# Kernel tuning notes

Hardware: AMD Instinct MI355X
Metric: run time of the kernel (lower is better)

## Reference

```python
import jax, jax.numpy as jnp
import numpy as np

# Hyperparameters (from TopoGradLoss.__init__)
K_KDE = 32      # neighbors for the Gaussian KDE density estimate
K_RIPS = 16     # neighbors defining the Rips (k-NN) graph
SCALE = 64.0    # Gaussian kernel bandwidth (squared-distance scale)
DESTNUM = 10    # number of salient persistence pairs to preserve
N, D = 8192, 32


def setup_inputs() -> dict:
    key = jax.random.key(0)
    x = jax.random.normal(key, (N, D), dtype=jnp.float32)
    return {"x": x}


def _kde_and_rips(x):
    # Full pairwise squared distances [N, N] (memory-bound traffic)
    sq = jnp.sum(x * x, axis=1)
    d2 = jnp.maximum(sq[:, None] + sq[None, :] - 2.0 * (x @ x.T), 0.0)
    # KDE density from the K_KDE nearest neighbors (self included, exp(0))
    neg_knn, _ = jax.lax.top_k(-d2, K_KDE)          # negated smallest sq-dists
    kde = jnp.exp(neg_knn / SCALE).sum(axis=1)       # sum_j exp(-||xi-xj||^2/scale)
    kde = kde / kde.max()                            # normalize to max density 1
    # Rips graph: K_RIPS nearest-neighbor indices
    _, rips_idxs = jax.lax.top_k(-d2, K_RIPS)
    return kde, rips_idxs


def _persistence_pairs(kde, rips_idxs):
    # ToMATo-style 0-dim persistence of the superlevel-set filtration of kde
    # on the k-NN Rips graph. Process points in decreasing density; each new
    # point either starts a cluster or merges clusters, killing all but the
    # densest root. death[r] = index of the point at which cluster born at r dies.
    n = kde.shape[0]
    order = jnp.argsort(-kde)     # decreasing density
    rank = jnp.argsort(order)     # rank[i] = filtration position of point i

    def step(carry, i):
        root, death = carry
        nbr = rips_idxs[i]                          # [K_RIPS]
        valid = rank[nbr] < rank[i]                 # neighbors already in filtration
        nroot = root[nbr]                           # their current cluster roots
        scores = jnp.where(valid, kde[nroot], -jnp.inf)
        g = jnp.where(valid.any(), nroot[jnp.argmax(scores)], i)  # surviving root
        # roots that die at point i (merged into g)
        dying = jnp.where(valid & (nroot != g), nroot, n)
        death = death.at[dying].set(i, mode="drop")
        # re-root every point whose root got merged
        merge_from = jnp.where(valid, nroot, -1)
        member = (root[:, None] == merge_from[None, :]).any(axis=1)
        root = jnp.where(member, g, root).at[i].set(g)
        return (root, death), None

    root0 = jnp.arange(n)
    death0 = jnp.full((n,), -1, dtype=jnp.int32)
    (root, death), _ = jax.lax.scan(step, (root0, death0), order)
    # essential pair: global density mode paired with the global minimum
    death = death.at[order[0]].set(jnp.argmin(kde).astype(death.dtype))
    return death


def _loss(kde, death):
    valid = death >= 0
    dvals = kde[jnp.clip(death, 0)]                 # death densities
    pers = kde - dvals                              # persistence per birth index
    masked = jnp.where(valid, jax.lax.stop_gradient(pers), -jnp.inf)
    _, top_idx = jax.lax.top_k(masked, DESTNUM)     # DESTNUM most persistent pairs
    salient = jnp.zeros(kde.shape[0], dtype=bool).at[top_idx].set(True)
    changing = valid & ~salient
    # collapse spurious pairs to zero persistence
    l_change = jnp.sum(jnp.where(changing, pers ** 2, 0.0))
    # push salient pairs toward maximal saliency (birth=1, death=0)
    l_salient = jnp.sum(jnp.where(valid & salient, (kde - 1.0) ** 2 + dvals ** 2, 0.0))
    return l_change + l_salient


def reference(x):
    kde, rips_idxs = _kde_and_rips(x)
    # pairing is combinatorial: piecewise-constant w.r.t. x (stop-gradient),
    # matching the custom autograd Function's gradient semantics
    death = _persistence_pairs(jax.lax.stop_gradient(kde), rips_idxs)
    return _loss(kde, death)
```

## Files before the change

kernel.cpp:

```cpp
#include <hip/hip_runtime.h>
#include <hip/hip_bf16.h>

#define NPTS 8192
#define DIM 32
#define KKDE 32
#define KRIPS 16
#define DESTNUM 10

__device__ __forceinline__ unsigned long long shfl_xor_u64(unsigned long long v, int m) {
  int lo = __shfl_xor((int)(unsigned)(v & 0xFFFFFFFFull), m, 64);
  int hi = __shfl_xor((int)(unsigned)(v >> 32), m, 64);
  return (((unsigned long long)(unsigned)hi) << 32) | (unsigned)lo;
}

template <int CTRL>
__device__ __forceinline__ int dpp_mov(int v) {
  return __builtin_amdgcn_update_dpp(0, v, CTRL, 0xF, 0xF, false);
}
__device__ __forceinline__ int row_max16(int v) {
  int t;
  t = dpp_mov<0x128>(v); v = (t > v) ? t : v;
  t = dpp_mov<0x124>(v); v = (t > v) ? t : v;
  t = dpp_mov<0x122>(v); v = (t > v) ? t : v;
  t = dpp_mov<0x121>(v); v = (t > v) ? t : v;
  return v;
}
__device__ __forceinline__ int row_min16(int v) {
  int t;
  t = dpp_mov<0x128>(v); v = (t < v) ? t : v;
  t = dpp_mov<0x124>(v); v = (t < v) ? t : v;
  t = dpp_mov<0x122>(v); v = (t < v) ? t : v;
  t = dpp_mov<0x121>(v); v = (t < v) ? t : v;
  return v;
}
__device__ __forceinline__ int wave_sum64(int c) {
  int t;
  t = dpp_mov<0x128>(c); c += t;
  t = dpp_mov<0x124>(c); c += t;
  t = dpp_mov<0x122>(c); c += t;
  t = dpp_mov<0x121>(c); c += t;
  return __builtin_amdgcn_readlane(c, 0) + __builtin_amdgcn_readlane(c, 16) +
         __builtin_amdgcn_readlane(c, 32) + __builtin_amdgcn_readlane(c, 48);
}

__global__ __launch_bounds__(64) void detect_kernel(const unsigned short* __restrict__ x,
                                                    int* __restrict__ flag) {
  int lane = threadIdx.x;
  unsigned u = x[2 * lane];
  int e = (u >> 7) & 0xFF;
  bool pass = (e >= 110 && e <= 130);
  unsigned long long b = __ballot(pass);
  if (lane == 0) flag[0] = (__popcll(b) >= 32) ? 1 : 0;
}

__global__ __launch_bounds__(256) void tr_kernel(const unsigned short* __restrict__ xh,
                                                 const int* __restrict__ flag,
                                                 float* __restrict__ xT) {
  int e = blockIdx.x * 256 + threadIdx.x;
  if (e >= NPTS * DIM) return;
  int p = e >> 5, q = e & 31;
  float v;
  if (flag[0] != 0) v = __uint_as_float(((unsigned)xh[e]) << 16);
  else v = ((const float*)xh)[e];
  xT[q * NPTS + p] = v;
}

__device__ __forceinline__ void topk_emit(const unsigned* K, const int i, const int w,
                                          const int lane, const int t,
                                          unsigned long long* cand, unsigned long long* srt,
                                          unsigned long long* fin, float* knnv, int* knni,
                                          float* __restrict__ kde, int* __restrict__ rips) {
  unsigned lo = 0u, hi = 0x7F800000u;
  int chi = 2048;
  while (chi > 64 && (hi - lo) > 3u) {
    const unsigned span = hi - lo;
    const unsigned t1 = lo + (span >> 2);
    const unsigned t2 = lo + (span >> 1);
    int c = 0;
#pragma unroll
    for (int e = 0; e < 32; ++e) {
      unsigned a = (K[e] <= t2) ? 0x10000u : 0u;
      a = (K[e] <= t1) ? 0x10001u : a;
      c += (int)a;
    }
    const int tot = wave_sum64(c);
    const int c1 = tot & 0xFFFF;
    const int c2 = (int)((unsigned)tot >> 16);
    if (c1 >= 32) { hi = t1; chi = c1; }
    else if (c2 >= 32) { lo = t1; hi = t2; chi = c2; }
    else lo = t2;
  }
  while (chi > 64 && (hi - lo) > 1u) {
    const unsigned mid = lo + ((hi - lo) >> 1);
    int c = 0;
#pragma unroll
    for (int e = 0; e < 32; ++e) c += (K[e] <= mid) ? 1 : 0;
    const int tot = wave_sum64(c);
    if (tot >= 32) { hi = mid; chi = tot; } else lo = mid;
  }
  cand[(w << 6) | lane] = ~0ull;
  const unsigned long long below = (lane == 0) ? 0ull : (~0ull >> (64 - lane));
  int base = 0;
#pragma unroll
  for (int e = 0; e < 32; ++e) {
    const bool sel = (K[e] <= hi);
    const unsigned long long b = __ballot(sel);
    if (sel) {
      const int pos = base + __popcll(b & below);
      if (pos < 64) {
        const int col = ((((w << 9) + ((e >> 2) << 6) + lane)) << 2) + (e & 3);
        cand[(w << 6) + pos] = (((unsigned long long)K[e]) << 32) | (unsigned)col;
      }
    }
    base += __popcll(b);
  }
  unsigned long long v = cand[(w << 6) | lane];
#pragma unroll
  for (int k = 2; k <= 64; k <<= 1) {
#pragma unroll
    for (int j = 32; j > 0; j >>= 1) {
      if (j >= k) continue;
      unsigned long long o = shfl_xor_u64(v, j);
      bool keepMin = (((lane & k) == 0) == ((lane & j) == 0));
      v = keepMin ? (v < o ? v : o) : (v > o ? v : o);
    }
  }
  if (lane < 32) srt[(w << 5) | lane] = v;
  __syncthreads();
  if (w < 2) {
    const unsigned long long* A = &srt[(w * 2) << 5];
    const unsigned long long* B = &srt[(w * 2 + 1) << 5];
    unsigned long long m = (lane < 32) ? A[lane] : B[63 - lane];
#pragma unroll
    for (int j = 32; j > 0; j >>= 1) {
      unsigned long long o = shfl_xor_u64(m, j);
      bool keepMin = ((lane & j) == 0);
      m = keepMin ? (m < o ? m : o) : (m > o ? m : o);
    }
    if (lane < 32) fin[(w << 5) | lane] = m;
  }
  __syncthreads();
  if (w == 0) {
    unsigned long long m = (lane < 32) ? fin[lane] : fin[32 + (63 - lane)];
#pragma unroll
    for (int j = 32; j > 0; j >>= 1) {
      unsigned long long o = shfl_xor_u64(m, j);
      bool keepMin = ((lane & j) == 0);
      m = keepMin ? (m < o ? m : o) : (m > o ? m : o);
    }
    if (lane < 32) {
      knnv[lane] = __uint_as_float((unsigned)(m >> 32));
      knni[lane] = (int)(m & 0x1FFFull);
    }
  }
  __syncthreads();
  if (t == 0) {
    float s = 0.f;
    for (int k = 0; k < KKDE; ++k) s += expf(knnv[k] * -0.015625f);
    kde[i] = s;
  }
  if (t < KRIPS) rips[i * KRIPS + t] = knni[t];
}

__global__ __launch_bounds__(256) void dist_kernel(const float* __restrict__ xT,
                                                   float* __restrict__ Dc,
                                                   int c0) {
  __shared__ float ax[DIM][128];
  __shared__ float bx[DIM][128];
  __shared__ float sqS[128];
  __shared__ float sS[128];
  const int t = threadIdx.x;
  const int i0 = c0 + blockIdx.y * 128;
  const int j0 = blockIdx.x * 128;
  for (int e = t; e < DIM * 128; e += 256) {
    int q = e >> 7, l = e & 127;
    ax[q][l] = xT[q * NPTS + i0 + l];
    bx[q][l] = xT[q * NPTS + j0 + l];
  }
  __syncthreads();
  {
    const int l = t & 127;
    const float* col = (t < 128) ? &ax[0][l] : &bx[0][l];
    float s = 0.f;
#pragma unroll
    for (int q = 0; q < DIM; ++q) s = fmaf(col[q * 128], col[q * 128], s);
    if (t < 128) sqS[l] = s;
    else sS[l] = s;
  }
  __syncthreads();
  const int tr = (t >> 4) << 3;
  const int tc = (t & 15) << 3;
  float acc[8][8];
#pragma unroll
  for (int a = 0; a < 8; ++a)
#pragma unroll
    for (int b = 0; b < 8; ++b) acc[a][b] = 0.f;
#pragma unroll 4
  for (int q = 0; q < DIM; ++q) {
    float4 a0 = *(const float4*)&ax[q][tr];
    float4 a1 = *(const float4*)&ax[q][tr + 4];
    float4 b0 = *(const float4*)&bx[q][tc];
    float4 b1 = *(const float4*)&bx[q][tc + 4];
    float ar[8] = {a0.x, a0.y, a0.z, a0.w, a1.x, a1.y, a1.z, a1.w};
    float br[8] = {b0.x, b0.y, b0.z, b0.w, b1.x, b1.y, b1.z, b1.w};
#pragma unroll
    for (int a = 0; a < 8; ++a)
#pragma unroll
      for (int b = 0; b < 8; ++b) acc[a][b] = fmaf(ar[a], br[b], acc[a][b]);
  }
#pragma unroll
  for (int a = 0; a < 8; ++a) {
    const float sqi = sqS[tr + a];
    float4 o0, o1;
    o0.x = fmaxf(fmaf(-2.f, acc[a][0], sqi + sS[tc + 0]), 0.f);
    o0.y = fmaxf(fmaf(-2.f, acc[a][1], sqi + sS[tc + 1]), 0.f);
    o0.z = fmaxf(fmaf(-2.f, acc[a][2], sqi + sS[tc + 2]), 0.f);
    o0.w = fmaxf(fmaf(-2.f, acc[a][3], sqi + sS[tc + 3]), 0.f);
    o1.x = fmaxf(fmaf(-2.f, acc[a][4], sqi + sS[tc + 4]), 0.f);
    o1.y = fmaxf(fmaf(-2.f, acc[a][5], sqi + sS[tc + 5]), 0.f);
    o1.z = fmaxf(fmaf(-2.f, acc[a][6], sqi + sS[tc + 6]), 0.f);
    o1.w = fmaxf(fmaf(-2.f, acc[a][7], sqi + sS[tc + 7]), 0.f);
    float* dst = Dc + (size_t)(i0 - c0 + tr + a) * NPTS + (j0 + tc);
    *(float4*)dst = o0;
    *(float4*)(dst + 4) = o1;
  }
}

__global__ __launch_bounds__(256) void select_kernel(const float* __restrict__ Dc,
                                                     float* __restrict__ kde,
                                                     int* __restrict__ rips,
                                                     int c0) {
  __shared__ unsigned long long cand[4 * 64];
  __shared__ unsigned long long srt[4 * 32];
  __shared__ unsigned long long fin[64];
  __shared__ float knnv[KKDE];
  __shared__ int knni[KKDE];
  const int i = c0 + blockIdx.x;
  const int t = threadIdx.x;
  const int w = t >> 6, lane = t & 63;
  const float4* D4 = (const float4*)(Dc + (size_t)blockIdx.x * NPTS);
  unsigned K[32];
#pragma unroll
  for (int s = 0; s < 8; ++s) {
    float4 v = D4[(w << 9) + (s << 6) + lane];
    K[4 * s + 0] = __float_as_uint(v.x);
    K[4 * s + 1] = __float_as_uint(v.y);
    K[4 * s + 2] = __float_as_uint(v.z);
    K[4 * s + 3] = __float_as_uint(v.w);
  }
  topk_emit(K, i, w, lane, t, cand, srt, fin, knnv, knni, kde, rips);
}

__global__ __launch_bounds__(256) void knn_kernel(const float* __restrict__ xT,
                                                  float* __restrict__ kde,
                                                  int* __restrict__ rips) {
  __shared__ unsigned long long cand[4 * 64];
  __shared__ unsigned long long srt[4 * 32];
  __shared__ unsigned long long fin[64];
  __shared__ float knnv[KKDE];
  __shared__ int knni[KKDE];
  __shared__ float xis[DIM];
  const int i = blockIdx.x;
  const int t = threadIdx.x;
  const int w = t >> 6, lane = t & 63;
  if (t < DIM) xis[t] = xT[t * NPTS + i];
  __syncthreads();
  float xi[DIM];
#pragma unroll
  for (int q = 0; q < DIM; ++q) xi[q] = xis[q];
  float sqi = 0.f;
#pragma unroll
  for (int q = 0; q < DIM; ++q) sqi = fmaf(xi[q], xi[q], sqi);
  const float4* xT4 = (const float4*)xT;
  unsigned K[32];
#pragma unroll
  for (int s = 0; s < 8; ++s) {
    const int j4 = (w << 9) + (s << 6) + lane;
    float d0 = 0.f, d1 = 0.f, d2 = 0.f, d3 = 0.f;
    float s0 = 0.f, s1 = 0.f, s2 = 0.f, s3 = 0.f;
#pragma unroll
    for (int q = 0; q < DIM; ++q) {
      float4 v = xT4[q * (NPTS / 4) + j4];
      const float xq = xi[q];
      d0 = fmaf(xq, v.x, d0); s0 = fmaf(v.x, v.x, s0);
      d1 = fmaf(xq, v.y, d1); s1 = fmaf(v.y, v.y, s1);
      d2 = fmaf(xq, v.z, d2); s2 = fmaf(v.z, v.z, s2);
      d3 = fmaf(xq, v.w, d3); s3 = fmaf(v.w, v.w, s3);
    }
    K[4 * s + 0] = __float_as_uint(fmaxf(fmaf(-2.f, d0, sqi + s0), 0.f));
    K[4 * s + 1] = __float_as_uint(fmaxf(fmaf(-2.f, d1, sqi + s1), 0.f));
    K[4 * s + 2] = __float_as_uint(fmaxf(fmaf(-2.f, d2, sqi + s2), 0.f));
    K[4 * s + 3] = __float_as_uint(fmaxf(fmaf(-2.f, d3, sqi + s3), 0.f));
  }
  topk_emit(K, i, w, lane, t, cand, srt, fin, knnv, knni, kde, rips);
}

__global__ __launch_bounds__(256) void prep_kernel(float* __restrict__ kde,
                                                   int* __restrict__ death,
                                                   int* __restrict__ scali) {
  __shared__ float red[256];
  __shared__ unsigned long long red64[256];
  __shared__ float kmaxS;
  const int t = threadIdx.x;
  float m = 0.f;
  for (int p = t; p < NPTS; p += 256) m = fmaxf(m, kde[p]);
  red[t] = m;
  __syncthreads();
  for (int s = 128; s; s >>= 1) {
    if (t < s) red[t] = fmaxf(red[t], red[t + s]);
    __syncthreads();
  }
  if (t == 0) kmaxS = red[0];
  __syncthreads();
  const float km = kmaxS;
  unsigned long long best = ~0ull;
  for (int p = t; p < NPTS; p += 256) {
    float v = kde[p] / km;
    kde[p] = v;
    death[p] = -1;
    unsigned long long kk = (((unsigned long long)__float_as_uint(v)) << 32) | (unsigned)p;
    if (kk < best) best = kk;
  }
  red64[t] = best;
  __syncthreads();
  for (int s = 128; s; s >>= 1) {
    if (t < s && red64[t + s] < red64[t]) red64[t] = red64[t + s];
    __syncthreads();
  }
  if (t == 0) scali[0] = (int)(red64[0] & 0xFFFFFFFFull);
}

__global__ __launch_bounds__(1024) void sort_kernel(const float* __restrict__ kde,
                                                    int* __restrict__ order,
                                                    int* __restrict__ rankp) {
  __shared__ float kv[NPTS];
  __shared__ unsigned short ki[NPTS];
  int t = threadIdx.x;
  for (int p = t; p < NPTS; p += 1024) { kv[p] = kde[p]; ki[p] = (unsigned short)p; }
  __syncthreads();
  for (int size = 2; size <= NPTS; size <<= 1) {
    for (int stride = size >> 1; stride > 0; stride >>= 1) {
      for (int q = t; q < NPTS / 2; q += 1024) {
        int lo = ((q & ~(stride - 1)) << 1) | (q & (stride - 1));
        int hi = lo + stride;
        float va = kv[lo], vb = kv[hi];
        int ia = ki[lo], ib = ki[hi];
        bool aFirst = (va > vb) || (va == vb && ia < ib);
        bool up = ((lo & size) == 0);
        if (up != aFirst) {
          kv[lo] = vb; kv[hi] = va;
          ki[lo] = (unsigned short)ib; ki[hi] = (unsigned short)ia;
        }
      }
      __syncthreads();
    }
  }
  for (int p = t; p < NPTS; p += 1024) {
    int idx = ki[p];
    order[p] = idx;
    rankp[idx] = p;
  }
}

__global__ __launch_bounds__(256) void onbr_kernel(const int* __restrict__ order,
                                                   const int* __restrict__ rankp,
                                                   const int* __restrict__ rips,
                                                   unsigned short* __restrict__ onbr) {
  int e = blockIdx.x * 256 + threadIdx.x;
  if (e >= NPTS * KRIPS) return;
  int t = e >> 4, kk = e & 15;
  int i = order[t];
  int nbr = rips[i * KRIPS + kk];
  int r = rankp[nbr];
  unsigned short v = (unsigned short)r;
  if (r < t) {
    v |= 0x8000;
    if ((r >> 4) == (t >> 4)) v |= 0x4000;
  }
  onbr[e] = v;
}

__global__ __launch_bounds__(64) void scan_kernel(const int* __restrict__ order,
                                                  const unsigned short* __restrict__ onbr,
                                                  int* __restrict__ death,
                                                  const int* __restrict__ scali) {
  __shared__ unsigned short rootR[NPTS];
  __shared__ unsigned short orderS[NPTS];
  const int lane = threadIdx.x;
  for (int p = lane; p < NPTS; p += 64) {
    rootR[p] = (unsigned short)p;
    orderS[p] = (unsigned short)order[p];
  }
  __syncthreads();
  const int sub = lane >> 4;

  auto process = [&](unsigned short D, int pref, int posBase, bool& cln) {
    const int nbr = D & 0x1FFF;
    const bool valid = (D & 0x8000) != 0;
    const bool hz = (D & 0x4000) != 0;
    int rd = cln ? pref : (int)rootR[nbr];
    const int rv = row_max16(valid ? rd : -1);
    const bool uniOk = !valid || (rd == rv);
    const unsigned long long uniB = __ballot(uniOk);
    const unsigned long long hzB = __ballot(hz);
    const unsigned long long badB = (~uniB) | hzB;
    if (badB == 0ull) {
      if ((lane & 15) == 0 && rv >= 0) rootR[posBase + sub] = (unsigned short)rv;
      return;
    }
    const int sstar = (__ffsll(badB) - 1) >> 4;
    if ((lane & 15) == 0 && sub < sstar && rv >= 0)
      rootR[posBase + sub] = (unsigned short)rv;
    cln = false;
    if (hzB != 0ull) {
      const int f = (int)rootR[nbr];
      rd = hz ? f : rd;
    }
    {
      const bool fwd2 = hz && (nbr >= posBase + sstar);
      const int rv2 = row_max16(valid ? rd : -1);
      const unsigned long long bad2 = __ballot(fwd2 || (valid && rd != rv2));
      if (bad2 == 0ull) {
        if ((lane & 15) == 0 && sub >= sstar && rv2 >= 0)
          rootR[posBase + sub] = (unsigned short)rv2;
        return;
      }
    }
    const unsigned long long vbAll = __ballot(valid);
    for (int s = sstar; s < 4; ++s) {
      const int pos = posBase + s;
      const unsigned long long smask = 0xFFFFull << (s << 4);
      const unsigned long long vb = vbAll & smask;
      if (vb == 0ull) continue;
      const int cl = __ffsll(vb) - 1;
      const int gc = __builtin_amdgcn_readlane(rd, cl);
      const unsigned long long uni2 = __ballot(!valid || rd == gc);
      if ((uni2 & smask) == smask) {
        if (lane == (s << 4)) rootR[pos] = (unsigned short)gc;
        if (nbr == pos) rd = gc;
      } else {
        const int g = __builtin_amdgcn_readlane(row_min16(valid ? rd : 0x7FFFFFFF), s << 4);
        const bool dy = (sub == s) && valid && (rd != g);
        if (dy) {
          const int pid = orderS[rd];
          rootR[rd] = (unsigned short)g;
          death[pid] = (int)orderS[pos];
        }
        if (lane == (s << 4)) rootR[pos] = (unsigned short)g;
        unsigned long long db = __ballot(dy);
        if (nbr == pos) rd = g;
        while (db != 0ull) {
          const int dl = __ffsll(db) - 1;
          const int rcX = __builtin_amdgcn_readlane(rd, dl);
          db &= ~__ballot(rd == rcX);
          for (int r = rcX + 1 + lane; r < pos; r += 64)
            if (rootR[r] == (unsigned short)rcX) rootR[r] = (unsigned short)g;
          if (rd == rcX) rd = g;
        }
      }
    }
  };

  unsigned short D0 = onbr[lane], D1 = onbr[64 + lane],
                 D2 = onbr[128 + lane], D3 = onbr[192 + lane];
  for (int b = 0; b < NPTS / 16; ++b) {
    unsigned short N0 = 0, N1 = 0, N2 = 0, N3 = 0;
    if (b + 1 < NPTS / 16) {
      const int nb = (b + 1) * 256 + lane;
      N0 = onbr[nb]; N1 = onbr[nb + 64]; N2 = onbr[nb + 128]; N3 = onbr[nb + 192];
    }
    const int p0 = (int)rootR[D0 & 0x1FFF];
    const int p1 = (int)rootR[D1 & 0x1FFF];
    const int p2 = (int)rootR[D2 & 0x1FFF];
    const int p3 = (int)rootR[D3 & 0x1FFF];
    bool cln = true;
    const int base = b << 4;
    process(D0, p0, base, cln);
    process(D1, p1, base + 4, cln);
    process(D2, p2, base + 8, cln);
    process(D3, p3, base + 12, cln);
    D0 = N0; D1 = N1; D2 = N2; D3 = N3;
  }
  if (lane == 0) death[orderS[0]] = scali[0];
}

__global__ __launch_bounds__(256) void loss_kernel(const float* __restrict__ kde,
                                                   const int* __restrict__ death,
                                                   float* __restrict__ out) {
  __shared__ float persS[NPTS];
  __shared__ float redv[256];
  __shared__ int redi[256];
  const int t = threadIdx.x;
  for (int p = t; p < NPTS; p += 256) {
    int d = death[p];
    persS[p] = (d < 0) ? -__builtin_inff() : kde[p] - kde[d];
  }
  __syncthreads();
  int chosen[DESTNUM];
  for (int k = 0; k < DESTNUM; ++k) {
    float bv = -__builtin_inff();
    int bi = 1 << 30;
    for (int p = t; p < NPTS; p += 256) {
      float pv = persS[p];
      if (pv > bv || (pv == bv && p < bi)) { bv = pv; bi = p; }
    }
    redv[t] = bv; redi[t] = bi;
    __syncthreads();
    for (int s = 128; s; s >>= 1) {
      if (t < s) {
        if (redv[t + s] > redv[t] || (redv[t + s] == redv[t] && redi[t + s] < redi[t])) {
          redv[t] = redv[t + s];
          redi[t] = redi[t + s];
        }
      }
      __syncthreads();
    }
    chosen[k] = redi[0];
    if (t == 0 && redi[0] < NPTS) persS[redi[0]] = -__builtin_inff();
    __syncthreads();
  }
  float acc = 0.f;
  for (int p = t; p < NPTS; p += 256) {
    int d = death[p];
    if (d < 0) continue;
    bool sal = false;
    for (int c = 0; c < DESTNUM; ++c) sal |= (chosen[c] == p);
    float dv = kde[d];
    float kp = kde[p];
    acc += sal ? ((kp - 1.f) * (kp - 1.f) + dv * dv) : (kp - dv) * (kp - dv);
  }
  redv[t] = acc;
  __syncthreads();
  for (int s = 128; s; s >>= 1) {
    if (t < s) redv[t] += redv[t + s];
    __syncthreads();
  }
  if (t == 0) out[0] = redv[0];
}

extern "C" void kernel_launch(void* const* d_in, const int* in_sizes, int n_in,
                              void* d_out, int out_size, void* d_ws, size_t ws_size,
                              hipStream_t stream) {
  const unsigned short* x = (const unsigned short*)d_in[0];

  float* xT = (float*)d_ws;
  float* kde = xT + NPTS * DIM;
  int* scali = (int*)(kde + NPTS);
  int* flag = scali + 64;
  int* order = flag + 64;
  int* rankp = order + NPTS;
  int* rips = rankp + NPTS;
  unsigned short* onbr = (unsigned short*)(rips + NPTS * KRIPS);
  int* death = (int*)(onbr + NPTS * KRIPS);

  size_t baseBytes = (size_t)((char*)(death + NPTS) - (char*)d_ws);
  baseBytes = (baseBytes + 1023) & ~(size_t)1023;
  float* Dc = (float*)((char*)d_ws + baseBytes);
  size_t avail = (ws_size > baseBytes) ? (ws_size - baseBytes) : 0;
  const size_t rowB = (size_t)NPTS * 4;
  int CH = 0;
  for (int c = NPTS; c >= 1024; c >>= 1)
    if (avail >= (size_t)c * rowB) { CH = c; break; }

  hipLaunchKernelGGL(detect_kernel, dim3(1), dim3(64), 0, stream, x, flag);
  hipLaunchKernelGGL(tr_kernel, dim3(NPTS * DIM / 256), dim3(256), 0, stream, x, flag, xT);
  if (CH > 0) {
    for (int c0 = 0; c0 < NPTS; c0 += CH) {
      hipLaunchKernelGGL(dist_kernel, dim3(NPTS / 128, CH / 128), dim3(256), 0, stream,
                         xT, Dc, c0);
      hipLaunchKernelGGL(select_kernel, dim3(CH), dim3(256), 0, stream, Dc, kde, rips, c0);
    }
  } else {
    hipLaunchKernelGGL(knn_kernel, dim3(NPTS), dim3(256), 0, stream, xT, kde, rips);
  }
  hipLaunchKernelGGL(prep_kernel, dim3(1), dim3(256), 0, stream, kde, death, scali);
  hipLaunchKernelGGL(sort_kernel, dim3(1), dim3(1024), 0, stream, kde, order, rankp);
  hipLaunchKernelGGL(onbr_kernel, dim3(NPTS * KRIPS / 256), dim3(256), 0, stream,
                     order, rankp, rips, onbr);
  hipLaunchKernelGGL(scan_kernel, dim3(1), dim3(64), 0, stream, order, onbr, death, scali);
  hipLaunchKernelGGL(loss_kernel, dim3(1), dim3(256), 0, stream, kde, death, (float*)d_out);
}
```

Baseline: 860.2 us.

## Batch root relabeling into one vectorized pass and widen single-block prep/loss kernels

```diff
diff --git a/kernel.cpp b/kernel.cpp
--- a/kernel.cpp
+++ b/kernel.cpp
@@ -295,18 +295,18 @@
   topk_emit(K, i, w, lane, t, cand, srt, fin, knnv, knni, kde, rips);
 }
 
-__global__ __launch_bounds__(256) void prep_kernel(float* __restrict__ kde,
-                                                   int* __restrict__ death,
-                                                   int* __restrict__ scali) {
-  __shared__ float red[256];
-  __shared__ unsigned long long red64[256];
+__global__ __launch_bounds__(1024) void prep_kernel(float* __restrict__ kde,
+                                                    int* __restrict__ death,
+                                                    int* __restrict__ scali) {
+  __shared__ float red[1024];
+  __shared__ unsigned long long red64[1024];
   __shared__ float kmaxS;
   const int t = threadIdx.x;
   float m = 0.f;
-  for (int p = t; p < NPTS; p += 256) m = fmaxf(m, kde[p]);
+  for (int p = t; p < NPTS; p += 1024) m = fmaxf(m, kde[p]);
   red[t] = m;
   __syncthreads();
-  for (int s = 128; s; s >>= 1) {
+  for (int s = 512; s; s >>= 1) {
     if (t < s) red[t] = fmaxf(red[t], red[t + s]);
     __syncthreads();
   }
@@ -314,7 +314,7 @@
   __syncthreads();
   const float km = kmaxS;
   unsigned long long best = ~0ull;
-  for (int p = t; p < NPTS; p += 256) {
+  for (int p = t; p < NPTS; p += 1024) {
     float v = kde[p] / km;
     kde[p] = v;
     death[p] = -1;
@@ -323,7 +323,7 @@
   }
   red64[t] = best;
   __syncthreads();
-  for (int s = 128; s; s >>= 1) {
+  for (int s = 512; s; s >>= 1) {
     if (t < s && red64[t + s] < red64[t]) red64[t] = red64[t + s];
     __syncthreads();
   }
@@ -384,7 +384,7 @@
                                                   const unsigned short* __restrict__ onbr,
                                                   int* __restrict__ death,
                                                   const int* __restrict__ scali) {
-  __shared__ unsigned short rootR[NPTS];
+  __shared__ __align__(16) unsigned short rootR[NPTS];
   __shared__ unsigned short orderS[NPTS];
   const int lane = threadIdx.x;
   for (int p = lane; p < NPTS; p += 64) {
@@ -447,15 +447,48 @@
           death[pid] = (int)orderS[pos];
         }
         if (lane == (s << 4)) rootR[pos] = (unsigned short)g;
+        const int mnr = __builtin_amdgcn_readlane(row_min16(dy ? rd : 0x7FFFFFFF), s << 4);
         unsigned long long db = __ballot(dy);
         if (nbr == pos) rd = g;
         while (db != 0ull) {
           const int dl = __ffsll(db) - 1;
           const int rcX = __builtin_amdgcn_readlane(rd, dl);
           db &= ~__ballot(rd == rcX);
-          for (int r = rcX + 1 + lane; r < pos; r += 64)
-            if (rootR[r] == (unsigned short)rcX) rootR[r] = (unsigned short)g;
           if (rd == rcX) rd = g;
+        }
+        {
+          const int c0 = (mnr + 1) >> 3;
+          const int c1 = (pos + 7) >> 3;
+          uint4* root4 = (uint4*)rootR;
+          const unsigned gg = (unsigned)g;
+          const unsigned um = (unsigned)mnr;
+          const unsigned lim = (unsigned)(pos - mnr);
+          for (int c = c0 + lane; c < c1; c += 64) {
+            uint4 vv = root4[c];
+            unsigned w0 = vv.x & 0xFFFFu, w1 = vv.x >> 16;
+            unsigned w2 = vv.y & 0xFFFFu, w3 = vv.y >> 16;
+            unsigned w4 = vv.z & 0xFFFFu, w5 = vv.z >> 16;
+            unsigned w6 = vv.w & 0xFFFFu, w7 = vv.w >> 16;
+            const bool h0 = (w0 - um) < lim, h1 = (w1 - um) < lim;
+            const bool h2 = (w2 - um) < lim, h3 = (w3 - um) < lim;
+            const bool h4 = (w4 - um) < lim, h5 = (w5 - um) < lim;
+            const bool h6 = (w6 - um) < lim, h7 = (w7 - um) < lim;
+            if (h0 | h1 | h2 | h3 | h4 | h5 | h6 | h7) {
+              if (h0 && rootR[w0] == (unsigned short)gg) w0 = gg;
+              if (h1 && rootR[w1] == (unsigned short)gg) w1 = gg;
+              if (h2 && rootR[w2] == (unsigned short)gg) w2 = gg;
+              if (h3 && rootR[w3] == (unsigned short)gg) w3 = gg;
+              if (h4 && rootR[w4] == (unsigned short)gg) w4 = gg;
+              if (h5 && rootR[w5] == (unsigned short)gg) w5 = gg;
+              if (h6 && rootR[w6] == (unsigned short)gg) w6 = gg;
+              if (h7 && rootR[w7] == (unsigned short)gg) w7 = gg;
+              vv.x = w0 | (w1 << 16);
+              vv.y = w2 | (w3 << 16);
+              vv.z = w4 | (w5 << 16);
+              vv.w = w6 | (w7 << 16);
+              root4[c] = vv;
+            }
+          }
         }
       }
     }
@@ -484,14 +517,14 @@
   if (lane == 0) death[orderS[0]] = scali[0];
 }
 
-__global__ __launch_bounds__(256) void loss_kernel(const float* __restrict__ kde,
-                                                   const int* __restrict__ death,
-                                                   float* __restrict__ out) {
+__global__ __launch_bounds__(1024) void loss_kernel(const float* __restrict__ kde,
+                                                    const int* __restrict__ death,
+                                                    float* __restrict__ out) {
   __shared__ float persS[NPTS];
-  __shared__ float redv[256];
-  __shared__ int redi[256];
+  __shared__ float redv[1024];
+  __shared__ int redi[1024];
   const int t = threadIdx.x;
-  for (int p = t; p < NPTS; p += 256) {
+  for (int p = t; p < NPTS; p += 1024) {
     int d = death[p];
     persS[p] = (d < 0) ? -__builtin_inff() : kde[p] - kde[d];
   }
@@ -500,13 +533,13 @@
   for (int k = 0; k < DESTNUM; ++k) {
     float bv = -__builtin_inff();
     int bi = 1 << 30;
-    for (int p = t; p < NPTS; p += 256) {
+    for (int p = t; p < NPTS; p += 1024) {
       float pv = persS[p];
       if (pv > bv || (pv == bv && p < bi)) { bv = pv; bi = p; }
     }
     redv[t] = bv; redi[t] = bi;
     __syncthreads();
-    for (int s = 128; s; s >>= 1) {
+    for (int s = 512; s; s >>= 1) {
       if (t < s) {
         if (redv[t + s] > redv[t] || (redv[t + s] == redv[t] && redi[t + s] < redi[t])) {
           redv[t] = redv[t + s];
@@ -520,7 +553,7 @@
     __syncthreads();
   }
   float acc = 0.f;
-  for (int p = t; p < NPTS; p += 256) {
+  for (int p = t; p < NPTS; p += 1024) {
     int d = death[p];
     if (d < 0) continue;
     bool sal = false;
@@ -531,7 +564,7 @@
   }
   redv[t] = acc;
   __syncthreads();
-  for (int s = 128; s; s >>= 1) {
+  for (int s = 512; s; s >>= 1) {
     if (t < s) redv[t] += redv[t + s];
     __syncthreads();
   }
@@ -573,10 +606,10 @@
   } else {
     hipLaunchKernelGGL(knn_kernel, dim3(NPTS), dim3(256), 0, stream, xT, kde, rips);
   }
-  hipLaunchKernelGGL(prep_kernel, dim3(1), dim3(256), 0, stream, kde, death, scali);
+  hipLaunchKernelGGL(prep_kernel, dim3(1), dim3(1024), 0, stream, kde, death, scali);
   hipLaunchKernelGGL(sort_kernel, dim3(1), dim3(1024), 0, stream, kde, order, rankp);
   hipLaunchKernelGGL(onbr_kernel, dim3(NPTS * KRIPS / 256), dim3(256), 0, stream,
                      order, rankp, rips, onbr);
   hipLaunchKernelGGL(scan_kernel, dim3(1), dim3(64), 0, stream, order, onbr, death, scali);
-  hipLaunchKernelGGL(loss_kernel, dim3(1), dim3(256), 0, stream, kde, death, (float*)d_out);
-}
+  hipLaunchKernelGGL(loss_kernel, dim3(1), dim3(1024), 0, stream, kde, death, (float*)d_out);
+}
```

Measured after the change: 833.2 us. 3.1% less time.
